# Performance work log

Measured on AMD Instinct MI355X. Metric: run time of the kernel, lower is better.

## Reference

```python
import jax, jax.numpy as jnp
import numpy as np

B, S, E, H = 4, 2048, 1024, 16
D = E // H
EPS = 1e-5
NEG = -1e9


def setup_inputs() -> dict:
    key = jax.random.key(0)
    ks = jax.random.split(key, 16)
    scale = 1.0 / np.sqrt(E)
    inp = {
        "q": jax.random.normal(ks[0], (B, S, E), jnp.float32),
        "k": jax.random.normal(ks[1], (B, S, E), jnp.float32),
        "v": jax.random.normal(ks[2], (B, S, E), jnp.float32),
        "mask": jax.random.randint(ks[3], (B, S, S), 0, 2).astype(bool),
        # Linear weights stored as (in, out); matches torch math with random init.
        "W1": jax.random.normal(ks[4], (E, E), jnp.float32) * scale,
        "b1": jnp.zeros((E,), jnp.float32),
        "W2": jax.random.normal(ks[5], (E, E), jnp.float32) * scale,
        "b2": jnp.zeros((E,), jnp.float32),
        "W3": jax.random.normal(ks[6], (E, E), jnp.float32) * scale,
        "b3": jnp.zeros((E,), jnp.float32),
        "W4": jax.random.normal(ks[7], (E, E), jnp.float32) * scale,
        "b4": jnp.zeros((E,), jnp.float32),
        "gamma": jnp.ones((E,), jnp.float32),
        "beta": jnp.zeros((E,), jnp.float32),
    }
    return inp


def _layer_norm(x, gamma, beta):
    mu = jnp.mean(x, axis=-1, keepdims=True)
    var = jnp.mean(jnp.square(x - mu), axis=-1, keepdims=True)
    return (x - mu) * jax.lax.rsqrt(var + EPS) * gamma + beta


def reference(q, k, v, mask, W1, b1, W2, b2, W3, b3, W4, b4, gamma, beta):
    vn = _layer_norm(v, gamma, beta)          # same LayerNorm params used twice
    residual = vn
    # projections -> [B, H, S, D]
    qh = (q @ W1 + b1).reshape(B, S, H, D).transpose(0, 2, 1, 3)
    kh = (k @ W2 + b2).reshape(B, S, H, D).transpose(0, 2, 1, 3)
    vh = (vn @ W3 + b3).reshape(B, S, H, D).transpose(0, 2, 1, 3)
    # NOTE: original module omits the 1/sqrt(D) scale -- keep it faithful.
    scores = jnp.einsum("bhqd,bhkd->bhqk", qh, kh)
    scores = jnp.where(mask[:, None, :, :], NEG, scores)
    attn = jax.nn.softmax(scores, axis=-1)
    out = jnp.einsum("bhqk,bhkd->bhqd", attn, vh)
    out = out.transpose(0, 2, 1, 3).reshape(B, S, E)
    out = out @ W4 + b4 + residual
    return _layer_norm(out, gamma, beta)
```

## Files before the change

kernel.cpp:

```cpp
#include <hip/hip_runtime.h>

typedef unsigned short u16;
typedef unsigned int u32;
typedef unsigned long long u64;
typedef float f32x4 __attribute__((ext_vector_type(4)));
typedef short short8 __attribute__((ext_vector_type(8)));
typedef short bf16x4 __attribute__((ext_vector_type(4)));

#define BB 4
#define SS 2048
#define EE 1024
#define HH 16
#define DD 64
#define EPSV 1e-5f
#define LOG2E 1.4426950408889634f

__device__ __forceinline__ u16 f2b(float x) {
  u32 u = __float_as_uint(x);
  u32 r = (u + 0x7fffu + ((u >> 16) & 1u)) >> 16;
  return (u16)r;
}
__device__ __forceinline__ float b2f(u16 u) {
  return __uint_as_float(((u32)u) << 16);
}
__device__ __forceinline__ u32 cvtpk(float lo, float hi) {
  u32 r;
  asm("v_cvt_pk_bf16_f32 %0, %1, %2" : "=v"(r) : "v"(lo), "v"(hi));
  return r;
}
__device__ __forceinline__ float fexp2(float x) {
  float r;
  asm("v_exp_f32 %0, %1" : "=v"(r) : "v"(x));
  return r;
}
__device__ __forceinline__ void gload16(const void* g, void* l) {
  __builtin_amdgcn_global_load_lds(
      (const __attribute__((address_space(1))) u32*)g,
      (__attribute__((address_space(3))) u32*)l, 16, 0, 0);
}
__device__ __forceinline__ f32x4 mfma16(bf16x4 a, bf16x4 b, f32x4 c) {
#if __has_builtin(__builtin_amdgcn_mfma_f32_16x16x16_bf16)
  return __builtin_amdgcn_mfma_f32_16x16x16_bf16(a, b, c, 0, 0, 0);
#elif __has_builtin(__builtin_amdgcn_mfma_f32_16x16x16bf16_1k)
  return __builtin_amdgcn_mfma_f32_16x16x16bf16_1k(a, b, c, 0, 0, 0);
#else
  asm("v_mfma_f32_16x16x16_bf16 %0, %1, %2, %3"
      : "=v"(c) : "v"(a), "v"(b), "v"(c));
  return c;
#endif
}

template<bool OUT_BF16>
__global__ __launch_bounds__(256) void ln_kernel(const float* __restrict__ x,
    const float* __restrict__ gamma, const float* __restrict__ beta,
    void* __restrict__ outp) {
  int row = blockIdx.x;
  int t = threadIdx.x;
  const float4* xr = (const float4*)(x + (size_t)row * EE);
  float4 v = xr[t];
  float s = v.x + v.y + v.z + v.w;
  #pragma unroll
  for (int o = 1; o < 64; o <<= 1) s += __shfl_xor(s, o);
  __shared__ float red[8];
  int wid = t >> 6;
  if ((t & 63) == 0) red[wid] = s;
  __syncthreads();
  float mean = (red[0] + red[1] + red[2] + red[3]) * (1.0f / EE);
  float d0 = v.x - mean, d1 = v.y - mean, d2 = v.z - mean, d3 = v.w - mean;
  float sq = d0 * d0 + d1 * d1 + d2 * d2 + d3 * d3;
  #pragma unroll
  for (int o = 1; o < 64; o <<= 1) sq += __shfl_xor(sq, o);
  if ((t & 63) == 0) red[4 + wid] = sq;
  __syncthreads();
  float var = (red[4] + red[5] + red[6] + red[7]) * (1.0f / EE);
  float rstd = rsqrtf(var + EPSV);
  float4 g = ((const float4*)gamma)[t];
  float4 be = ((const float4*)beta)[t];
  float o0 = d0 * rstd * g.x + be.x;
  float o1 = d1 * rstd * g.y + be.y;
  float o2 = d2 * rstd * g.z + be.z;
  float o3 = d3 * rstd * g.w + be.w;
  if (OUT_BF16) {
    ushort4 pk;
    pk.x = f2b(o0); pk.y = f2b(o1); pk.z = f2b(o2); pk.w = f2b(o3);
    *(ushort4*)((u16*)outp + (size_t)row * EE + t * 4) = pk;
  } else {
    ((float4*)((float*)outp + (size_t)row * EE))[t] = make_float4(o0, o1, o2, o3);
  }
}

__global__ __launch_bounds__(256) void pre_kernel(
    const float* __restrict__ v, const float* __restrict__ gamma,
    const float* __restrict__ beta, u16* __restrict__ vn,
    const float* __restrict__ q, u16* __restrict__ qbf,
    const float* __restrict__ k, u16* __restrict__ kbf,
    const int* __restrict__ mask, u64* __restrict__ mp,
    const float* __restrict__ W1, const float* __restrict__ W2,
    const float* __restrict__ W3, const float* __restrict__ W4,
    u16* __restrict__ W1t, u16* __restrict__ W2t,
    u16* __restrict__ W3t, u16* __restrict__ W4t) {
  __shared__ float tile[32][33];
  __shared__ float red[8];
  int idx = blockIdx.x;
  int t = threadIdx.x;
  if (idx < 8192) {
    int row = idx;
    float4 vv = ((const float4*)(v + (size_t)row * EE))[t];
    float s = vv.x + vv.y + vv.z + vv.w;
    #pragma unroll
    for (int o = 1; o < 64; o <<= 1) s += __shfl_xor(s, o);
    int wid = t >> 6;
    if ((t & 63) == 0) red[wid] = s;
    __syncthreads();
    float mean = (red[0] + red[1] + red[2] + red[3]) * (1.0f / EE);
    float d0 = vv.x - mean, d1 = vv.y - mean, d2 = vv.z - mean, d3 = vv.w - mean;
    float sq = d0 * d0 + d1 * d1 + d2 * d2 + d3 * d3;
    #pragma unroll
    for (int o = 1; o < 64; o <<= 1) sq += __shfl_xor(sq, o);
    if ((t & 63) == 0) red[4 + wid] = sq;
    __syncthreads();
    float var = (red[4] + red[5] + red[6] + red[7]) * (1.0f / EE);
    float rstd = rsqrtf(var + EPSV);
    float4 g = ((const float4*)gamma)[t];
    float4 be = ((const float4*)beta)[t];
    ushort4 pk;
    pk.x = f2b(d0 * rstd * g.x + be.x);
    pk.y = f2b(d1 * rstd * g.y + be.y);
    pk.z = f2b(d2 * rstd * g.z + be.z);
    pk.w = f2b(d3 * rstd * g.w + be.w);
    *(ushort4*)(vn + (size_t)row * EE + t * 4) = pk;
  } else if (idx < 16384) {
    int i = idx - 8192;
    const float* x = (i >= 4096) ? k : q;
    u16* y = (i >= 4096) ? kbf : qbf;
    size_t off = ((size_t)(i & 4095) * 256 + t) * 8;
    float4 a = *(const float4*)(x + off);
    float4 c = *(const float4*)(x + off + 4);
    uint4 pk;
    pk.x = (u32)f2b(a.x) | ((u32)f2b(a.y) << 16);
    pk.y = (u32)f2b(a.z) | ((u32)f2b(a.w) << 16);
    pk.z = (u32)f2b(c.x) | ((u32)f2b(c.y) << 16);
    pk.w = (u32)f2b(c.z) | ((u32)f2b(c.w) << 16);
    *(uint4*)(y + off) = pk;
  } else if (idx < 32768) {
    int widx = idx - 16384;
    int wv = t >> 6, lane = t & 63;
    size_t base = (size_t)widx * 1024 + wv * 256;
    int v0 = mask[base + 0 * 64 + lane];
    int v1 = mask[base + 1 * 64 + lane];
    int v2 = mask[base + 2 * 64 + lane];
    int v3 = mask[base + 3 * 64 + lane];
    u64 b0 = __ballot(v0 != 0);
    u64 b1 = __ballot(v1 != 0);
    u64 b2 = __ballot(v2 != 0);
    u64 b3 = __ballot(v3 != 0);
    if (lane == 0) {
      u64* dst = &mp[base >> 6];
      dst[0] = b0; dst[1] = b1; dst[2] = b2; dst[3] = b3;
    }
  } else {
    int s = idx - 32768;
    int w = s >> 10, t2 = s & 1023;
    int kb = (t2 & 31) * 32, nb = (t2 >> 5) * 32;
    const float* W = (w == 0) ? W1 : (w == 1) ? W2 : (w == 2) ? W3 : W4;
    u16* Wt = (w == 0) ? W1t : (w == 1) ? W2t : (w == 2) ? W3t : W4t;
    int r = t >> 3, c = (t & 7) * 4;
    float4 vv = *(const float4*)&W[(size_t)(kb + r) * EE + nb + c];
    tile[r][c] = vv.x; tile[r][c + 1] = vv.y;
    tile[r][c + 2] = vv.z; tile[r][c + 3] = vv.w;
    __syncthreads();
    uint2 val;
    val.x = (u32)f2b(tile[c][r]) | ((u32)f2b(tile[c + 1][r]) << 16);
    val.y = (u32)f2b(tile[c + 2][r]) | ((u32)f2b(tile[c + 3][r]) << 16);
    *(uint2*)&Wt[(size_t)(nb + r) * EE + kb + c] = val;
  }
}

__global__ __launch_bounds__(256) void gemm_proj(
    const u16* __restrict__ Aq, const u16* __restrict__ Ak,
    const u16* __restrict__ Av,
    const u16* __restrict__ W1t, const u16* __restrict__ W2t,
    const u16* __restrict__ W3t,
    const float* __restrict__ b1, const float* __restrict__ b2,
    const float* __restrict__ b3,
    u16* __restrict__ qh, u16* __restrict__ kh, u16* __restrict__ vt,
    int yoff) {
  constexpr int N = 1024, K = 1024;
  __shared__ u16 Al[128 * 32];
  __shared__ u16 Bl[128 * 32];
  int y = blockIdx.y + yoff;
  int sel = y >> 6, my = y & 63;
  const u16* Ap = (sel == 0) ? Aq : (sel == 1) ? Ak : Av;
  const u16* Bt = (sel == 0) ? W1t : (sel == 1) ? W2t : W3t;
  const float* bias = (sel == 0) ? b1 : (sel == 1) ? b2 : b3;
  u16* Cp = (sel == 0) ? qh : (sel == 1) ? kh : vt;
  float oscale = (sel == 0) ? LOG2E : 1.0f;

  int t = threadIdx.x;
  int lane = t & 63, wid = t >> 6;
  int mb = my * 128, nb = blockIdx.x * 128;
  int wm = (wid >> 1) * 64, wn = (wid & 1) * 64;
  int l15 = lane & 15, lg = lane >> 4;

  int srow = lane >> 2;
  int schunk = (lane & 3) ^ (srow & 3);
  const u16* Ag = Ap + (size_t)(mb + wid * 32 + srow) * K + schunk * 8;
  const u16* Bg = Bt + (size_t)(nb + wid * 32 + srow) * K + schunk * 8;
  u16* Alw0 = &Al[(wid * 32) * 32];
  u16* Alw1 = &Al[(wid * 32 + 16) * 32];
  u16* Blw0 = &Bl[(wid * 32) * 32];
  u16* Blw1 = &Bl[(wid * 32 + 16) * 32];
  int ca = (lg ^ (l15 & 3)) * 8;

  f32x4 acc[4][4] = {};
  for (int kt = 0; kt < K; kt += 32) {
    gload16(Ag + kt, Alw0);
    gload16(Ag + kt + (size_t)16 * K, Alw1);
    gload16(Bg + kt, Blw0);
    gload16(Bg + kt + (size_t)16 * K, Blw1);
    __syncthreads();
    short8 af[4], bfv[4];
    #pragma unroll
    for (int mf = 0; mf < 4; mf++)
      af[mf] = *(const short8*)&Al[(wm + mf * 16 + l15) * 32 + ca];
    #pragma unroll
    for (int nf = 0; nf < 4; nf++)
      bfv[nf] = *(const short8*)&Bl[(wn + nf * 16 + l15) * 32 + ca];
    #pragma unroll
    for (int mf = 0; mf < 4; mf++)
      #pragma unroll
      for (int nf = 0; nf < 4; nf++)
        acc[mf][nf] = __builtin_amdgcn_mfma_f32_16x16x32_bf16(af[mf], bfv[nf], acc[mf][nf], 0, 0, 0);
    __syncthreads();
  }
  float bv[4];
  #pragma unroll
  for (int nf = 0; nf < 4; nf++) bv[nf] = bias[nb + wn + nf * 16 + l15];
  if (sel == 2) {
    #pragma unroll
    for (int mf = 0; mf < 4; mf++) {
      int m0 = mb + wm + mf * 16 + lg * 4;
      int bq = m0 >> 11, s0 = m0 & 2047;
      #pragma unroll
      for (int nf = 0; nf < 4; nf++) {
        int n = nb + wn + nf * 16 + l15;
        int h = n >> 6, d = n & 63;
        ushort4 pk;
        pk.x = f2b(acc[mf][nf][0] + bv[nf]);
        pk.y = f2b(acc[mf][nf][1] + bv[nf]);
        pk.z = f2b(acc[mf][nf][2] + bv[nf]);
        pk.w = f2b(acc[mf][nf][3] + bv[nf]);
        *(ushort4*)&vt[((size_t)((bq * HH + h) * DD + d)) * SS + s0] = pk;
      }
    }
  } else {
    #pragma unroll
    for (int mf = 0; mf < 4; mf++) {
      #pragma unroll
      for (int r = 0; r < 4; r++) {
        int m = mb + wm + mf * 16 + lg * 4 + r;
        #pragma unroll
        for (int nf = 0; nf < 4; nf++) {
          int n = nb + wn + nf * 16 + l15;
          Cp[(size_t)m * N + n] = f2b((acc[mf][nf][r] + bv[nf]) * oscale);
        }
      }
    }
  }
}

__global__ __launch_bounds__(256) void gemm_out(const u16* __restrict__ Ap,
    const u16* __restrict__ Bt, const float* __restrict__ bias,
    const u16* __restrict__ resid, float* __restrict__ Cp) {
  constexpr int N = 1024, K = 1024;
  __shared__ u16 Al[128 * 32];
  __shared__ u16 Bl[128 * 32];
  int t = threadIdx.x;
  int lane = t & 63, wid = t >> 6;
  int mb = blockIdx.y * 128, nb = blockIdx.x * 128;
  int wm = (wid >> 1) * 64, wn = (wid & 1) * 64;
  int l15 = lane & 15, lg = lane >> 4;
  int srow = lane >> 2;
  int schunk = (lane & 3) ^ (srow & 3);
  const u16* Ag = Ap + (size_t)(mb + wid * 32 + srow) * K + schunk * 8;
  const u16* Bg = Bt + (size_t)(nb + wid * 32 + srow) * K + schunk * 8;
  u16* Alw0 = &Al[(wid * 32) * 32];
  u16* Alw1 = &Al[(wid * 32 + 16) * 32];
  u16* Blw0 = &Bl[(wid * 32) * 32];
  u16* Blw1 = &Bl[(wid * 32 + 16) * 32];
  int ca = (lg ^ (l15 & 3)) * 8;
  f32x4 acc[4][4] = {};
  for (int kt = 0; kt < K; kt += 32) {
    gload16(Ag + kt, Alw0);
    gload16(Ag + kt + (size_t)16 * K, Alw1);
    gload16(Bg + kt, Blw0);
    gload16(Bg + kt + (size_t)16 * K, Blw1);
    __syncthreads();
    short8 af[4], bfv[4];
    #pragma unroll
    for (int mf = 0; mf < 4; mf++)
      af[mf] = *(const short8*)&Al[(wm + mf * 16 + l15) * 32 + ca];
    #pragma unroll
    for (int nf = 0; nf < 4; nf++)
      bfv[nf] = *(const short8*)&Bl[(wn + nf * 16 + l15) * 32 + ca];
    #pragma unroll
    for (int mf = 0; mf < 4; mf++)
      #pragma unroll
      for (int nf = 0; nf < 4; nf++)
        acc[mf][nf] = __builtin_amdgcn_mfma_f32_16x16x32_bf16(af[mf], bfv[nf], acc[mf][nf], 0, 0, 0);
    __syncthreads();
  }
  float bv[4];
  #pragma unroll
  for (int nf = 0; nf < 4; nf++) bv[nf] = bias[nb + wn + nf * 16 + l15];
  #pragma unroll
  for (int mf = 0; mf < 4; mf++) {
    #pragma unroll
    for (int r = 0; r < 4; r++) {
      int m = mb + wm + mf * 16 + lg * 4 + r;
      #pragma unroll
      for (int nf = 0; nf < 4; nf++) {
        int n = nb + wn + nf * 16 + l15;
        float rv = b2f(resid[(size_t)m * N + n]);
        Cp[(size_t)m * N + n] = acc[mf][nf][r] + bv[nf] + rv;
      }
    }
  }
}

__global__ __launch_bounds__(256) void attn_kernel(const u16* __restrict__ qh,
    const u16* __restrict__ kh, const u16* __restrict__ vt,
    const u64* __restrict__ mp, u16* __restrict__ outp) {
  __shared__ u16 Kl[64 * 64];
  __shared__ u16 Vl[64 * 64];
  __shared__ u64 lutq[16];
  int t = threadIdx.x, lane = t & 63, wid = t >> 6;
  int bh = blockIdx.y, b = bh >> 4, h = bh & 15;
  int qt = blockIdx.x;
  int l15 = lane & 15, lg = lane >> 4;

  if (t < 16) {
    u32 n = t;
    u32 w0 = ((n & 1) ? 0u : 0xFFFFu) | ((n & 2) ? 0u : 0xFFFF0000u);
    u32 w1 = ((n & 4) ? 0u : 0xFFFFu) | ((n & 8) ? 0u : 0xFFFF0000u);
    lutq[n] = (u64)w0 | ((u64)w1 << 32);
  }

  int qrow = qt * 64 + wid * 16 + l15;
  const u16* qbase = qh + ((size_t)(b * SS + qrow)) * EE + h * DD;
  short8 qf0 = *(const short8*)(qbase + lg * 8);
  short8 qf1 = *(const short8*)(qbase + 32 + lg * 8);
  const u64* mrow = mp + (size_t)(b * SS + qrow) * (SS / 64);

  bf16x4 onesv;
  #pragma unroll
  for (int i = 0; i < 4; i++) onesv[i] = (short)0x3F80;

  int r0 = wid * 16 + (lane >> 3);
  int r1 = r0 + 8;
  int cc = lane & 7;
  int wk0 = r0 * 64 + ((cc ^ (r0 & 7)) * 8);
  int wk1 = r1 * 64 + ((cc ^ (r1 & 7)) * 8);
  const u16* kgb = kh + ((size_t)b * SS) * EE + h * DD;
  const u16* vgb = vt + ((size_t)bh * DD) * SS;

  int ck0 = (lg ^ (l15 & 7)) * 8;
  int ck1 = ((4 + lg) ^ (l15 & 7)) * 8;
  int vbase0 = l15 * 64 + ((lg >> 1) ^ (l15 & 7)) * 8 + (lg & 1) * 4;

  f32x4 O[4] = {};
  f32x4 asum = {};
  constexpr int NT = SS / 64;

  uint4 sk0 = *(const uint4*)(kgb + (size_t)r0 * EE + cc * 8);
  uint4 sk1 = *(const uint4*)(kgb + (size_t)r1 * EE + cc * 8);
  uint4 sv0 = *(const uint4*)(vgb + (size_t)r0 * SS + cc * 8);
  uint4 sv1 = *(const uint4*)(vgb + (size_t)r1 * SS + cc * 8);
  const u16* kp0 = kgb + (size_t)(64 + r0) * EE + cc * 8;
  const u16* kp1 = kgb + (size_t)(64 + r1) * EE + cc * 8;
  const u16* vp0 = vgb + (size_t)r0 * SS + 64 + cc * 8;
  const u16* vp1 = vgb + (size_t)r1 * SS + 64 + cc * 8;
  u64 mw = mrow[0];

  for (int kt = 0; kt < NT; ++kt) {
    *(uint4*)&Kl[wk0] = sk0;
    *(uint4*)&Kl[wk1] = sk1;
    *(uint4*)&Vl[wk0] = sv0;
    *(uint4*)&Vl[wk1] = sv1;
    __syncthreads();

    sk0 = *(const uint4*)kp0; kp0 += 64 * EE;
    sk1 = *(const uint4*)kp1; kp1 += 64 * EE;
    sv0 = *(const uint4*)vp0; vp0 += 64;
    sv1 = *(const uint4*)vp1; vp1 += 64;
    u64 mwn = mrow[kt + 1];

    u32 mlo = (u32)(mw >> (lg * 4));
    u32 mhi = (u32)(mw >> 32 >> (lg * 4));
    uint2 pat[4];
    pat[0] = *(uint2*)&lutq[mlo & 15u];
    pat[1] = *(uint2*)&lutq[(mlo >> 16) & 15u];
    pat[2] = *(uint2*)&lutq[mhi & 15u];
    pat[3] = *(uint2*)&lutq[(mhi >> 16) & 15u];

    f32x4 sc[4];
    #pragma unroll
    for (int nf = 0; nf < 4; nf++) {
      int row = nf * 16 + l15;
      short8 k0 = *(const short8*)&Kl[row * 64 + ck0];
      short8 k1 = *(const short8*)&Kl[row * 64 + ck1];
      f32x4 z = {};
      z = __builtin_amdgcn_mfma_f32_16x16x32_bf16(k0, qf0, z, 0, 0, 0);
      z = __builtin_amdgcn_mfma_f32_16x16x32_bf16(k1, qf1, z, 0, 0, 0);
      sc[nf] = z;
    }

    #pragma unroll
    for (int nf = 0; nf < 4; nf++) {
      #pragma unroll
      for (int r = 0; r < 4; r++)
        sc[nf][r] = fexp2(sc[nf][r]);
    }

    #pragma unroll
    for (int nf = 0; nf < 4; nf++) {
      bf16x4 pb;
      ((u32*)&pb)[0] = cvtpk(sc[nf][0], sc[nf][1]) & pat[nf].x;
      ((u32*)&pb)[1] = cvtpk(sc[nf][2], sc[nf][3]) & pat[nf].y;
      asum = mfma16(onesv, pb, asum);
      int vo = vbase0 ^ (nf * 16);
      #pragma unroll
      for (int df = 0; df < 4; df++) {
        bf16x4 vf = *(const bf16x4*)&Vl[vo + df * 1024];
        O[df] = mfma16(vf, pb, O[df]);
      }
    }
    mw = mwn;
    __syncthreads();
  }

  float inv = 1.0f / asum[0];
  u16* ob = outp + ((size_t)(b * SS + qrow)) * EE + h * DD + lg * 4;
  #pragma unroll
  for (int df = 0; df < 4; df++) {
    ushort4 pk;
    pk.x = f2b(O[df][0] * inv);
    pk.y = f2b(O[df][1] * inv);
    pk.z = f2b(O[df][2] * inv);
    pk.w = f2b(O[df][3] * inv);
    *(ushort4*)(ob + df * 16) = pk;
  }
}

extern "C" void kernel_launch(void* const* d_in, const int* in_sizes, int n_in,
                              void* d_out, int out_size, void* d_ws, size_t ws_size,
                              hipStream_t stream) {
  (void)in_sizes; (void)n_in; (void)out_size;
  const float* q    = (const float*)d_in[0];
  const float* k    = (const float*)d_in[1];
  const float* v    = (const float*)d_in[2];
  const int*   mask = (const int*)d_in[3];
  const float* W1   = (const float*)d_in[4];
  const float* b1   = (const float*)d_in[5];
  const float* W2   = (const float*)d_in[6];
  const float* b2   = (const float*)d_in[7];
  const float* W3   = (const float*)d_in[8];
  const float* b3   = (const float*)d_in[9];
  const float* W4   = (const float*)d_in[10];
  const float* b4   = (const float*)d_in[11];
  const float* gamma = (const float*)d_in[12];
  const float* beta  = (const float*)d_in[13];
  float* out = (float*)d_out;
  char* ws = (char*)d_ws;
  const size_t MB = 1024 * 1024;
  u16* qh  = (u16*)(ws + 0 * MB);
  u16* kh  = (u16*)(ws + 16 * MB);
  u16* vt  = (u16*)(ws + 32 * MB);
  u16* ao  = (u16*)(ws + 48 * MB);
  u16* vn  = (u16*)(ws + 64 * MB);
  u16* W1t = (u16*)(ws + 80 * MB);
  u16* W2t = (u16*)(ws + 82 * MB);
  u16* W3t = (u16*)(ws + 84 * MB);
  u16* W4t = (u16*)(ws + 86 * MB);
  u64* mp  = (u64*)(ws + 88 * MB);
  float* tmp = (float*)(ws + 0 * MB);
  u16* qbf = ao;

  bool ws_ok = ws_size >= 107 * MB;
  u16* kbf = ws_ok ? (u16*)(ws + 90 * MB) : vt;

  pre_kernel<<<36864, 256, 0, stream>>>(v, gamma, beta, vn, q, qbf, k, kbf,
                                        mask, mp, W1, W2, W3, W4,
                                        W1t, W2t, W3t, W4t);
  if (ws_ok) {
    gemm_proj<<<dim3(8, 192), 256, 0, stream>>>(qbf, kbf, vn, W1t, W2t, W3t,
                                                b1, b2, b3, qh, kh, vt, 0);
  } else {
    gemm_proj<<<dim3(8, 128), 256, 0, stream>>>(qbf, kbf, vn, W1t, W2t, W3t,
                                                b1, b2, b3, qh, kh, vt, 0);
    gemm_proj<<<dim3(8, 64), 256, 0, stream>>>(qbf, kbf, vn, W1t, W2t, W3t,
                                               b1, b2, b3, qh, kh, vt, 128);
  }
  attn_kernel<<<dim3(32, 64), 256, 0, stream>>>(qh, kh, vt, mp, ao);
  gemm_out<<<dim3(8, 64), 256, 0, stream>>>(ao, W4t, b4, vn, tmp);
  ln_kernel<false><<<8192, 256, 0, stream>>>(tmp, gamma, beta, out);
}
```

Measured before the change: 297.7 us.

## Process two query tiles per attention block to reuse staged K/V tiles

Each attention workgroup now handles 128 query rows instead of 64, with every wave computing two independent 16-row query fragments against the same K and V tiles in LDS. This halves the grid in the query dimension and halves global K/V loads and LDS staging per query row, while giving more independent MFMA work between barriers. It costs more registers for the second set of accumulators, which may lower occupancy, and leaves fewer blocks to spread across the CUs.

Measured after the change: 281.7 us. -5.4%, faster.

```diff
diff --git a/kernel.cpp b/kernel.cpp
--- a/kernel.cpp
+++ b/kernel.cpp
@@ -346,11 +346,16 @@
     lutq[n] = (u64)w0 | ((u64)w1 << 32);
   }
 
-  int qrow = qt * 64 + wid * 16 + l15;
-  const u16* qbase = qh + ((size_t)(b * SS + qrow)) * EE + h * DD;
-  short8 qf0 = *(const short8*)(qbase + lg * 8);
-  short8 qf1 = *(const short8*)(qbase + 32 + lg * 8);
-  const u64* mrow = mp + (size_t)(b * SS + qrow) * (SS / 64);
+  int qrow0 = qt * 128 + wid * 16 + l15;
+  int qrow1 = qrow0 + 64;
+  const u16* qbase0 = qh + ((size_t)(b * SS + qrow0)) * EE + h * DD;
+  const u16* qbase1 = qh + ((size_t)(b * SS + qrow1)) * EE + h * DD;
+  short8 qa0 = *(const short8*)(qbase0 + lg * 8);
+  short8 qa1 = *(const short8*)(qbase0 + 32 + lg * 8);
+  short8 qb0 = *(const short8*)(qbase1 + lg * 8);
+  short8 qb1 = *(const short8*)(qbase1 + 32 + lg * 8);
+  const u64* mrow0 = mp + (size_t)(b * SS + qrow0) * (SS / 64);
+  const u64* mrow1 = mp + (size_t)(b * SS + qrow1) * (SS / 64);
 
   bf16x4 onesv;
   #pragma unroll
@@ -368,8 +373,8 @@
   int ck1 = ((4 + lg) ^ (l15 & 7)) * 8;
   int vbase0 = l15 * 64 + ((lg >> 1) ^ (l15 & 7)) * 8 + (lg & 1) * 4;
 
-  f32x4 O[4] = {};
-  f32x4 asum = {};
+  f32x4 Oa[4] = {}, Ob[4] = {};
+  f32x4 asuma = {}, asumb = {};
   constexpr int NT = SS / 64;
 
   uint4 sk0 = *(const uint4*)(kgb + (size_t)r0 * EE + cc * 8);
@@ -380,7 +385,8 @@
   const u16* kp1 = kgb + (size_t)(64 + r1) * EE + cc * 8;
   const u16* vp0 = vgb + (size_t)r0 * SS + 64 + cc * 8;
   const u16* vp1 = vgb + (size_t)r1 * SS + 64 + cc * 8;
-  u64 mw = mrow[0];
+  u64 mwa = mrow0[0];
+  u64 mwb = mrow1[0];
 
   for (int kt = 0; kt < NT; ++kt) {
     *(uint4*)&Kl[wk0] = sk0;
@@ -393,62 +399,86 @@
     sk1 = *(const uint4*)kp1; kp1 += 64 * EE;
     sv0 = *(const uint4*)vp0; vp0 += 64;
     sv1 = *(const uint4*)vp1; vp1 += 64;
-    u64 mwn = mrow[kt + 1];
-
-    u32 mlo = (u32)(mw >> (lg * 4));
-    u32 mhi = (u32)(mw >> 32 >> (lg * 4));
-    uint2 pat[4];
-    pat[0] = *(uint2*)&lutq[mlo & 15u];
-    pat[1] = *(uint2*)&lutq[(mlo >> 16) & 15u];
-    pat[2] = *(uint2*)&lutq[mhi & 15u];
-    pat[3] = *(uint2*)&lutq[(mhi >> 16) & 15u];
-
-    f32x4 sc[4];
+    u64 mwan = mrow0[kt + 1];
+    u64 mwbn = mrow1[kt + 1];
+
+    u32 mloa = (u32)(mwa >> (lg * 4));
+    u32 mhia = (u32)(mwa >> 32 >> (lg * 4));
+    u32 mlob = (u32)(mwb >> (lg * 4));
+    u32 mhib = (u32)(mwb >> 32 >> (lg * 4));
+    uint2 pata[4], patb[4];
+    pata[0] = *(uint2*)&lutq[mloa & 15u];
+    pata[1] = *(uint2*)&lutq[(mloa >> 16) & 15u];
+    pata[2] = *(uint2*)&lutq[mhia & 15u];
+    pata[3] = *(uint2*)&lutq[(mhia >> 16) & 15u];
+    patb[0] = *(uint2*)&lutq[mlob & 15u];
+    patb[1] = *(uint2*)&lutq[(mlob >> 16) & 15u];
+    patb[2] = *(uint2*)&lutq[mhib & 15u];
+    patb[3] = *(uint2*)&lutq[(mhib >> 16) & 15u];
+
+    f32x4 sca[4], scb[4];
     #pragma unroll
     for (int nf = 0; nf < 4; nf++) {
       int row = nf * 16 + l15;
       short8 k0 = *(const short8*)&Kl[row * 64 + ck0];
       short8 k1 = *(const short8*)&Kl[row * 64 + ck1];
-      f32x4 z = {};
-      z = __builtin_amdgcn_mfma_f32_16x16x32_bf16(k0, qf0, z, 0, 0, 0);
-      z = __builtin_amdgcn_mfma_f32_16x16x32_bf16(k1, qf1, z, 0, 0, 0);
-      sc[nf] = z;
+      f32x4 za = {}, zb = {};
+      za = __builtin_amdgcn_mfma_f32_16x16x32_bf16(k0, qa0, za, 0, 0, 0);
+      za = __builtin_amdgcn_mfma_f32_16x16x32_bf16(k1, qa1, za, 0, 0, 0);
+      zb = __builtin_amdgcn_mfma_f32_16x16x32_bf16(k0, qb0, zb, 0, 0, 0);
+      zb = __builtin_amdgcn_mfma_f32_16x16x32_bf16(k1, qb1, zb, 0, 0, 0);
+      sca[nf] = za;
+      scb[nf] = zb;
     }
 
     #pragma unroll
     for (int nf = 0; nf < 4; nf++) {
       #pragma unroll
-      for (int r = 0; r < 4; r++)
-        sc[nf][r] = fexp2(sc[nf][r]);
+      for (int r = 0; r < 4; r++) {
+        sca[nf][r] = fexp2(sca[nf][r]);
+        scb[nf][r] = fexp2(scb[nf][r]);
+      }
     }
 
     #pragma unroll
     for (int nf = 0; nf < 4; nf++) {
-      bf16x4 pb;
-      ((u32*)&pb)[0] = cvtpk(sc[nf][0], sc[nf][1]) & pat[nf].x;
-      ((u32*)&pb)[1] = cvtpk(sc[nf][2], sc[nf][3]) & pat[nf].y;
-      asum = mfma16(onesv, pb, asum);
+      bf16x4 pba, pbb;
+      ((u32*)&pba)[0] = cvtpk(sca[nf][0], sca[nf][1]) & pata[nf].x;
+      ((u32*)&pba)[1] = cvtpk(sca[nf][2], sca[nf][3]) & pata[nf].y;
+      ((u32*)&pbb)[0] = cvtpk(scb[nf][0], scb[nf][1]) & patb[nf].x;
+      ((u32*)&pbb)[1] = cvtpk(scb[nf][2], scb[nf][3]) & patb[nf].y;
+      asuma = mfma16(onesv, pba, asuma);
+      asumb = mfma16(onesv, pbb, asumb);
       int vo = vbase0 ^ (nf * 16);
       #pragma unroll
       for (int df = 0; df < 4; df++) {
         bf16x4 vf = *(const bf16x4*)&Vl[vo + df * 1024];
-        O[df] = mfma16(vf, pb, O[df]);
+        Oa[df] = mfma16(vf, pba, Oa[df]);
+        Ob[df] = mfma16(vf, pbb, Ob[df]);
       }
     }
-    mw = mwn;
-    __syncthreads();
-  }
-
-  float inv = 1.0f / asum[0];
-  u16* ob = outp + ((size_t)(b * SS + qrow)) * EE + h * DD + lg * 4;
+    mwa = mwan;
+    mwb = mwbn;
+    __syncthreads();
+  }
+
+  float inva = 1.0f / asuma[0];
+  float invb = 1.0f / asumb[0];
+  u16* ob0 = outp + ((size_t)(b * SS + qrow0)) * EE + h * DD + lg * 4;
+  u16* ob1 = outp + ((size_t)(b * SS + qrow1)) * EE + h * DD + lg * 4;
   #pragma unroll
   for (int df = 0; df < 4; df++) {
-    ushort4 pk;
-    pk.x = f2b(O[df][0] * inv);
-    pk.y = f2b(O[df][1] * inv);
-    pk.z = f2b(O[df][2] * inv);
-    pk.w = f2b(O[df][3] * inv);
-    *(ushort4*)(ob + df * 16) = pk;
+    ushort4 pka, pkb;
+    pka.x = f2b(Oa[df][0] * inva);
+    pka.y = f2b(Oa[df][1] * inva);
+    pka.z = f2b(Oa[df][2] * inva);
+    pka.w = f2b(Oa[df][3] * inva);
+    pkb.x = f2b(Ob[df][0] * invb);
+    pkb.y = f2b(Ob[df][1] * invb);
+    pkb.z = f2b(Ob[df][2] * invb);
+    pkb.w = f2b(Ob[df][3] * invb);
+    *(ushort4*)(ob0 + df * 16) = pka;
+    *(ushort4*)(ob1 + df * 16) = pkb;
   }
 }
 
@@ -501,7 +531,7 @@
     gemm_proj<<<dim3(8, 64), 256, 0, stream>>>(qbf, kbf, vn, W1t, W2t, W3t,
                                                b1, b2, b3, qh, kh, vt, 128);
   }
-  attn_kernel<<<dim3(32, 64), 256, 0, stream>>>(qh, kh, vt, mp, ao);
+  attn_kernel<<<dim3(16, 64), 256, 0, stream>>>(qh, kh, vt, mp, ao);
   gemm_out<<<dim3(8, 64), 256, 0, stream>>>(ao, W4t, b4, vn, tmp);
   ln_kernel<false><<<8192, 256, 0, stream>>>(tmp, gamma, beta, out);
 }
```
